# Performance work log

Measured on AMD Instinct MI355X. Metric: run time of the kernel, lower is better.

## Reference

```python
import jax, jax.numpy as jnp
import numpy as np

D_MODEL = 256
SEQ_L = 4096
BATCH = 8
H = 3 * D_MODEL   # inner width after 3-branch concat
N_STATE = 32      # complex conjugate pairs -> d_state=64 real
KSIZES = (3, 7, 15)
DILATIONS = (1, 2, 4)


def setup_inputs() -> dict:
    k = jax.random.split(jax.random.key(0), 16)
    d = D_MODEL
    def w(ki, shape, scale):
        return jax.random.normal(ki, shape, jnp.float32) * scale
    inp = {"x": jax.random.normal(k[0], (BATCH, SEQ_L, d), jnp.float32)}
    for i, ksz in enumerate(KSIZES):
        inp[f"conv_w{i}"] = w(k[1 + i], (d, d, ksz), (d * ksz) ** -0.5)
        inp[f"conv_b{i}"] = jnp.zeros((d,), jnp.float32)
    inp["gate_w"] = w(k[4], (H, d), d ** -0.5)
    inp["gate_b"] = jnp.zeros((H,), jnp.float32)
    inp["res_w"] = w(k[5], (H, d), d ** -0.5)
    inp["res_b"] = jnp.zeros((H,), jnp.float32)
    # S4D (diagonal SSM) parameters, d_state=64 -> 32 complex pairs
    inp["log_dt"] = jax.random.uniform(k[6], (H,), jnp.float32, np.log(0.001), np.log(0.1))
    inp["A_re"] = -0.5 * jnp.ones((H, N_STATE), jnp.float32)
    inp["A_im"] = jnp.broadcast_to(np.pi * jnp.arange(N_STATE, dtype=jnp.float32), (H, N_STATE)).copy()
    inp["C_re"] = w(k[7], (H, N_STATE), 0.2)
    inp["C_im"] = w(k[8], (H, N_STATE), 0.2)
    inp["Dskip"] = jax.random.normal(k[9], (H,), jnp.float32)
    inp["ln_gamma"] = jnp.ones((H,), jnp.float32)
    inp["ln_beta"] = jnp.zeros((H,), jnp.float32)
    return inp


def _dil_conv(u, w, b, dil):
    # u: [B, C, L], w: [O, I, K], torch 'same' padding (odd kernels)
    y = jax.lax.conv_general_dilated(
        u, w, window_strides=(1,), padding="SAME", rhs_dilation=(dil,),
        dimension_numbers=("NCH", "OIH", "NCH"))
    return y + b[None, :, None]


def _s4d_apply(u, log_dt, A_re, A_im, C_re, C_im, Dskip):
    # u: [B, H, L]; diagonal SSM long convolution via FFT (ZOH discretization)
    L = u.shape[-1]
    dt = jnp.exp(log_dt)                          # [H]
    A = A_re + 1j * A_im                          # [H, N]
    C = C_re + 1j * C_im                          # [H, N]
    dtA = dt[:, None] * A                         # [H, N]
    C_disc = C * (jnp.exp(dtA) - 1.0) / A         # ZOH input matrix folded into C
    t = jnp.arange(L, dtype=jnp.float32)
    vand = jnp.exp(dtA[:, :, None] * t)           # [H, N, L] Vandermonde
    kern = 2.0 * jnp.real(jnp.einsum("hn,hnl->hl", C_disc, vand))  # [H, L]
    n_fft = 2 * L
    kf = jnp.fft.rfft(kern, n_fft)                # [H, n_fft/2+1]
    uf = jnp.fft.rfft(u, n_fft)                   # [B, H, n_fft/2+1]
    y = jnp.fft.irfft(uf * kf[None], n_fft)[..., :L]
    return y + Dskip[None, :, None] * u


def reference(x, conv_w0, conv_b0, conv_w1, conv_b1, conv_w2, conv_b2,
              gate_w, gate_b, res_w, res_b,
              log_dt, A_re, A_im, C_re, C_im, Dskip, ln_gamma, ln_beta):
    u = jnp.transpose(x, (0, 2, 1))               # [B, d, L]
    convs = [
        _dil_conv(u, conv_w0, conv_b0, DILATIONS[0]),
        _dil_conv(u, conv_w1, conv_b1, DILATIONS[1]),
        _dil_conv(u, conv_w2, conv_b2, DILATIONS[2]),
    ]
    combined = jnp.concatenate(convs, axis=1)     # [B, 3d, L]
    gate = jax.nn.sigmoid(jnp.einsum("bdl,od->bol", u, gate_w) + gate_b[None, :, None])
    gated = combined * gate
    s4_out = _s4d_apply(gated, log_dt, A_re, A_im, C_re, C_im, Dskip)
    resid = jnp.einsum("bdl,od->bol", u, res_w) + res_b[None, :, None]
    out = jnp.transpose(s4_out + resid, (0, 2, 1))  # [B, L, 3d]
    mu = jnp.mean(out, axis=-1, keepdims=True)
    var = jnp.mean((out - mu) ** 2, axis=-1, keepdims=True)
    return (out - mu) * jax.lax.rsqrt(var + 1e-5) * ln_gamma + ln_beta
```

## Files before the change

kernel.cpp:

```cpp
#include <hip/hip_runtime.h>
#include <cstdint>
#include <cstddef>


#define B_ 8
#define L_ 4096
#define D_ 256
#define H_ 768
#define NST 32
#define LC 128
#define NC 32

typedef _Float16 f16;
typedef _Float16 f16x8 __attribute__((ext_vector_type(8)));
typedef _Float16 f16x4 __attribute__((ext_vector_type(4)));
typedef float f32x4 __attribute__((ext_vector_type(4)));

__device__ __forceinline__ f32x4 mfma16(f16x8 a, f16x8 b, f32x4 c) {
  return __builtin_amdgcn_mfma_f32_16x16x32_f16(a, b, c, 0, 0, 0);
}

#define GLDS16(g, l)                                                              \
  __builtin_amdgcn_global_load_lds((const __attribute__((address_space(1))) void*)(g), \
                                   (__attribute__((address_space(3))) void*)(l), 16, 0, 0)


__global__ __launch_bounds__(256) void cast4(const float* __restrict__ s, f16* __restrict__ d) {
  int i = (blockIdx.x * 256 + threadIdx.x) * 4;
  float4 x = *(const float4*)(s + i);
  d[i + 0] = (f16)x.x; d[i + 1] = (f16)x.y; d[i + 2] = (f16)x.z; d[i + 3] = (f16)x.w;
}

__global__ __launch_bounds__(256) void zfill(float* __restrict__ z) {
  z[threadIdx.x] = 0.f;
}

__global__ __launch_bounds__(256) void prep_convA(const float* __restrict__ w0,
                                                  const float* __restrict__ w1,
                                                  const float* __restrict__ w2,
                                                  f16* __restrict__ A) {
  int idx = blockIdx.x * 256 + threadIdx.x;
  const int n0 = 256 * 256 * 3, n1 = 256 * 256 * 7;
  const float* w; int K, base;
  if (idx < n0) { w = w0; K = 3; base = 0; }
  else if (idx < n0 + n1) { idx -= n0; w = w1; K = 7; base = 256 * 768; }
  else { idx -= n0 + n1; w = w2; K = 15; base = 256 * 768 + 256 * 1792; }
  int o = idx / (256 * K); int r = idx - o * (256 * K); int j = r / K; int t = r - j * K;
  A[base + o * (256 * K) + t * 256 + j] = (f16)w[idx];
}

__global__ __launch_bounds__(256) void s4_params(const float* __restrict__ log_dt,
                                                 const float* __restrict__ A_re,
                                                 const float* __restrict__ A_im,
                                                 const float* __restrict__ C_re,
                                                 const float* __restrict__ C_im,
                                                 f16* __restrict__ A1, f16* __restrict__ A2,
                                                 float* __restrict__ WLc) {
  int idx = blockIdx.x * 256 + threadIdx.x;
  int h = idx >> 5, n = idx & 31;
  float dt = expf(log_dt[h]);
  float Ar = A_re[idx], Ai = A_im[idx];
  float ar = dt * Ar, ai = dt * Ai;
  float e = expf(ar), sn, cs; sincosf(ai, &sn, &cs);
  float wr = e * cs, wi = e * sn;
  float den = Ar * Ar + Ai * Ai;
  float Er = wr - 1.f, Ei = wi;
  float Cr = C_re[idx], Ci = C_im[idx];
  float nr = Cr * Er - Ci * Ei, ni = Cr * Ei + Ci * Er;
  float Cdr = (nr * Ar + ni * Ai) / den;
  float Cdi = (ni * Ar - nr * Ai) / den;
  f16* A1r = A1 + ((size_t)h * 64 + 2 * n) * LC;
  f16* A1i = A1 + ((size_t)h * 64 + 2 * n + 1) * LC;
  float pr = 1.f, pi = 0.f;
  for (int j = 0; j < LC; ++j) {
    A1r[LC - 1 - j] = (f16)pr; A1i[LC - 1 - j] = (f16)pi;
    float t0 = pr * wr - pi * wi; pi = pr * wi + pi * wr; pr = t0;
  }
  WLc[idx * 2] = pr; WLc[idx * 2 + 1] = pi;
  float qr = wr, qi = wi;
  for (int t = 0; t < LC; ++t) {
    A2[((size_t)h * LC + t) * 64 + 2 * n]     = (f16)(2.f * (Cdr * qr - Cdi * qi));
    A2[((size_t)h * LC + t) * 64 + 2 * n + 1] = (f16)(-2.f * (Cdr * qi + Cdi * qr));
    float t0 = qr * wr - qi * wi; qi = qr * wi + qi * wr; qr = t0;
  }
}

__global__ __launch_bounds__(256) void s4_kernelvec(const float* __restrict__ log_dt,
                                                    const float* __restrict__ A_re,
                                                    const float* __restrict__ A_im,
                                                    const float* __restrict__ C_re,
                                                    const float* __restrict__ C_im,
                                                    float* __restrict__ kT) {
  int idx = blockIdx.x * 256 + threadIdx.x;
  int h = idx >> 7, j = idx & 127;
  float dt = expf(log_dt[h]);
  float acc = 0.f;
  for (int n = 0; n < NST; ++n) {
    float Ar = A_re[h * 32 + n], Ai = A_im[h * 32 + n];
    float ar = dt * Ar, ai = dt * Ai;
    float e1 = expf(ar), s1, c1; sincosf(ai, &s1, &c1);
    float wr = e1 * c1, wi = e1 * s1;
    float den = Ar * Ar + Ai * Ai;
    float Er = wr - 1.f, Ei = wi;
    float Cr = C_re[h * 32 + n], Ci = C_im[h * 32 + n];
    float nr = Cr * Er - Ci * Ei, ni = Cr * Ei + Ci * Er;
    float Cdr = (nr * Ar + ni * Ai) / den, Cdi = (ni * Ar - nr * Ai) / den;
    float ej = expf(ar * (float)j), sj, cj; sincosf(ai * (float)j, &sj, &cj);
    acc += 2.f * (Cdr * (ej * cj) - Cdi * (ej * sj));
  }
  kT[idx] = acc;
}

__global__ __launch_bounds__(256) void gemm_gr(
    const f16* __restrict__ xh, const f16* __restrict__ Agr,
    const float* __restrict__ gate_b, const float* __restrict__ res_b,
    f16* __restrict__ gts, f16* __restrict__ res) {
  __shared__ f16 As[128 * 64];
  __shared__ f16 Bs[128 * 64];
  const int mt = blockIdx.y, nt = blockIdx.x;
  const int b = nt >> 5, l0 = (nt & 31) * 128;
  const bool isg = mt < 6;
  const int hbase = (isg ? mt : mt - 6) * 128;
  const f16* Abase = Agr + (size_t)((isg ? 0 : 768) + hbase) * 256;
  const int tid = threadIdx.x;
  const int wid = tid >> 6, lane = tid & 63, l15 = lane & 15, quad = lane >> 4;
  const int wm = (wid & 1) * 64, wn = (wid >> 1) * 64;
  const int srow = (wid << 5) + (lane >> 3);
  const int sperm = ((lane & 7) ^ (lane >> 3)) << 3;
  char* AsL = (char*)As + (wid << 12);
  char* BsL = (char*)Bs + (wid << 12);
  const f16* xrow = xh + (((size_t)b * L_) << 8);

  f32x4 acc[4][4];
#pragma unroll
  for (int i = 0; i < 4; ++i)
#pragma unroll
    for (int j = 0; j < 4; ++j) acc[i][j] = (f32x4){0.f, 0.f, 0.f, 0.f};

  for (int kc = 0; kc < 4; ++kc) {
#pragma unroll
    for (int j = 0; j < 4; ++j) {
      int row = srow + j * 8;
      GLDS16(Abase + (size_t)row * 256 + kc * 64 + sperm, AsL + (j << 10));
      GLDS16(xrow + ((size_t)(l0 + row) << 8) + kc * 64 + sperm, BsL + (j << 10));
    }
    __syncthreads();
#pragma unroll
    for (int k2 = 0; k2 < 2; ++k2) {
      f16x8 af[4], bf[4];
#pragma unroll
      for (int mi = 0; mi < 4; ++mi) {
        int r = wm + mi * 16 + l15;
        af[mi] = *(const f16x8*)(&As[r * 64 + (((k2 * 4 + quad) ^ (r & 7)) << 3)]);
      }
#pragma unroll
      for (int ni = 0; ni < 4; ++ni) {
        int r = wn + ni * 16 + l15;
        bf[ni] = *(const f16x8*)(&Bs[r * 64 + (((k2 * 4 + quad) ^ (r & 7)) << 3)]);
      }
#pragma unroll
      for (int mi = 0; mi < 4; ++mi)
#pragma unroll
        for (int ni = 0; ni < 4; ++ni) acc[mi][ni] = mfma16(af[mi], bf[ni], acc[mi][ni]);
    }
    __syncthreads();
  }

  if (isg) {
#pragma unroll
    for (int mi = 0; mi < 4; ++mi)
#pragma unroll
      for (int ni = 0; ni < 4; ++ni) {
        int hg = hbase + wm + mi * 16 + quad * 4;
        int lg = l0 + wn + ni * 16 + l15;
#pragma unroll
        for (int r = 0; r < 4; ++r) {
          float val = acc[mi][ni][r] + gate_b[hg + r];
          gts[((size_t)(b * H_ + hg + r)) * L_ + lg] = (f16)(1.f / (1.f + expf(-val)));
        }
      }
  } else {
#pragma unroll
    for (int mi = 0; mi < 4; ++mi)
#pragma unroll
      for (int ni = 0; ni < 4; ++ni) {
        int hg = hbase + wm + mi * 16 + quad * 4;
        int lg = l0 + wn + ni * 16 + l15;
#pragma unroll
        for (int r = 0; r < 4; ++r)
          res[((size_t)(b * H_ + hg + r)) * L_ + lg] = (f16)(acc[mi][ni][r] + res_b[hg + r]);
      }
  }
}

__global__ __launch_bounds__(256) void gemm_conv(
    const f16* __restrict__ xh, const f16* __restrict__ Aconv,
    const float* __restrict__ cb0, const float* __restrict__ cb1, const float* __restrict__ cb2,
    const f16* __restrict__ gts, const f16* __restrict__ zbuf,
    f16* __restrict__ v) {
  __shared__ f16 As[128 * 64];
  __shared__ f16 Bs[128 * 64];
  const int mt = blockIdx.y, nt = blockIdx.x;
  const int b = nt >> 5, l0 = (nt & 31) * 128;
  const int ci = 2 - (mt >> 1);
  const int m0 = (mt & 1) * 128;
  const int tid = threadIdx.x;
  const int wid = tid >> 6, lane = tid & 63, l15 = lane & 15, quad = lane >> 4;
  const int wm = (wid & 1) * 64, wn = (wid >> 1) * 64;
  const int srow = (wid << 5) + (lane >> 3);
  const int sperm = ((lane & 7) ^ (lane >> 3)) << 3;
  char* AsL = (char*)As + (wid << 12);
  char* BsL = (char*)Bs + (wid << 12);
  const f16* xrow = xh + (((size_t)b * L_) << 8);

  const f16* Acb; int Krow, taps, dil;
  if (ci == 0)      { Acb = Aconv;                          Krow = 768;  taps = 3;  dil = 1; }
  else if (ci == 1) { Acb = Aconv + 256 * 768;              Krow = 1792; taps = 7;  dil = 2; }
  else              { Acb = Aconv + 256 * 768 + 256 * 1792; Krow = 3840; taps = 15; dil = 4; }

  f32x4 acc[4][4];
#pragma unroll
  for (int i = 0; i < 4; ++i)
#pragma unroll
    for (int j = 0; j < 4; ++j) acc[i][j] = (f32x4){0.f, 0.f, 0.f, 0.f};

  for (int t = 0; t < taps; ++t) {
    const f16* Arows = Acb + (size_t)m0 * Krow + t * 256;
    int boff = (t - (taps - 1) / 2) * dil;
    for (int kc = 0; kc < 4; ++kc) {
#pragma unroll
      for (int j = 0; j < 4; ++j) {
        int row = srow + j * 8;
        GLDS16(Arows + (size_t)row * Krow + kc * 64 + sperm, AsL + (j << 10));
        int gl = l0 + row + boff;
        const f16* gb = xrow + ((size_t)gl << 8) + kc * 64 + sperm;
        if (gl < 0 || gl >= L_) gb = zbuf;
        GLDS16(gb, BsL + (j << 10));
      }
      __syncthreads();
#pragma unroll
      for (int k2 = 0; k2 < 2; ++k2) {
        f16x8 af[4], bf[4];
#pragma unroll
        for (int mi = 0; mi < 4; ++mi) {
          int r = wm + mi * 16 + l15;
          af[mi] = *(const f16x8*)(&As[r * 64 + (((k2 * 4 + quad) ^ (r & 7)) << 3)]);
        }
#pragma unroll
        for (int ni = 0; ni < 4; ++ni) {
          int r = wn + ni * 16 + l15;
          bf[ni] = *(const f16x8*)(&Bs[r * 64 + (((k2 * 4 + quad) ^ (r & 7)) << 3)]);
        }
#pragma unroll
        for (int mi = 0; mi < 4; ++mi)
#pragma unroll
          for (int ni = 0; ni < 4; ++ni) acc[mi][ni] = mfma16(af[mi], bf[ni], acc[mi][ni]);
      }
      __syncthreads();
    }
  }

  const float* cbias = (ci == 0) ? cb0 : (ci == 1 ? cb1 : cb2);
#pragma unroll
  for (int mi = 0; mi < 4; ++mi)
#pragma unroll
    for (int ni = 0; ni < 4; ++ni) {
      int mg = m0 + wm + mi * 16 + quad * 4;
      int lg = l0 + wn + ni * 16 + l15;
#pragma unroll
      for (int r = 0; r < 4; ++r) {
        size_t a = ((size_t)(b * H_ + ci * 256 + mg + r)) * L_ + lg;
        float val = (acc[mi][ni][r] + cbias[mg + r]) * (float)gts[a];
        v[a] = (f16)val;
      }
    }
}

__global__ __launch_bounds__(256) void s1_states(const f16* __restrict__ v,
                                                 const f16* __restrict__ A1,
                                                 float* __restrict__ Xend) {
  __shared__ f16 A1s[64 * 136];
  __shared__ f16 Vs[128 * 136];
  const int h = blockIdx.y, cb = blockIdx.x;
  const int tid = threadIdx.x;
  {
    int row = tid >> 2, q = tid & 3;
    const f16x8* src = (const f16x8*)(A1 + ((size_t)h * 64 + row) * 128 + q * 32);
    f16x8* dst = (f16x8*)(&A1s[row * 136 + q * 32]);
    dst[0] = src[0]; dst[1] = src[1]; dst[2] = src[2]; dst[3] = src[3];
  }
  {
    int col = tid >> 1, half = tid & 1;
    int cg = cb * 128 + col, b = cg >> 5, c = cg & 31;
    const f16x8* src = (const f16x8*)(v + ((size_t)(b * H_ + h)) * L_ + c * 128 + half * 64);
    f16x8* dst = (f16x8*)(&Vs[col * 136 + half * 64]);
    dst[0] = src[0]; dst[1] = src[1]; dst[2] = src[2]; dst[3] = src[3];
    dst[4] = src[4]; dst[5] = src[5]; dst[6] = src[6]; dst[7] = src[7];
  }
  __syncthreads();
  const int wid = tid >> 6, lane = tid & 63, l15 = lane & 15, quad = lane >> 4;
  const int n0 = wid * 32;
  f32x4 acc[4][2];
#pragma unroll
  for (int i = 0; i < 4; ++i) { acc[i][0] = (f32x4){0,0,0,0}; acc[i][1] = (f32x4){0,0,0,0}; }
#pragma unroll
  for (int bk = 0; bk < 4; ++bk) {
    f16x8 af[4], bf[2];
#pragma unroll
    for (int mi = 0; mi < 4; ++mi)
      af[mi] = *(const f16x8*)(&A1s[(mi * 16 + l15) * 136 + bk * 32 + quad * 8]);
#pragma unroll
    for (int ni = 0; ni < 2; ++ni)
      bf[ni] = *(const f16x8*)(&Vs[(n0 + ni * 16 + l15) * 136 + bk * 32 + quad * 8]);
#pragma unroll
    for (int mi = 0; mi < 4; ++mi)
#pragma unroll
      for (int ni = 0; ni < 2; ++ni) acc[mi][ni] = mfma16(af[mi], bf[ni], acc[mi][ni]);
  }
#pragma unroll
  for (int mi = 0; mi < 4; ++mi)
#pragma unroll
    for (int ni = 0; ni < 2; ++ni) {
      int cg = cb * 128 + n0 + ni * 16 + l15, b = cg >> 5, c = cg & 31;
      float* dst = Xend + (((size_t)(b * H_ + h)) * NC + c) * 64 + mi * 16 + quad * 4;
      *(f32x4*)dst = acc[mi][ni];
    }
}

__global__ __launch_bounds__(256) void s2_scan(float* __restrict__ X, const float* __restrict__ WLc) {
  int idx = blockIdx.x * 256 + threadIdx.x;
  int n = idx & 31, bh = idx >> 5, h = bh % H_;
  float Wr = WLc[(h * NST + n) * 2], Wi = WLc[(h * NST + n) * 2 + 1];
  float xr = 0.f, xi = 0.f;
  float* base = X + (size_t)bh * NC * 64 + 2 * n;
  for (int c = 0; c < NC; ++c) {
    float er = base[c * 64], ei = base[c * 64 + 1];
    base[c * 64] = xr; base[c * 64 + 1] = xi;
    float t = Wr * xr - Wi * xi + er;
    xi = Wr * xi + Wi * xr + ei; xr = t;
  }
}

__global__ __launch_bounds__(256) void s3_output(const f16* __restrict__ v,
                                                 const f16* __restrict__ A2g,
                                                 const f16* __restrict__ res,
                                                 const float* __restrict__ kT,
                                                 const float* __restrict__ Xin,
                                                 const float* __restrict__ Dskip,
                                                 f16* __restrict__ y4) {
  __shared__ f16 Ts[128 * 136];
  __shared__ f16 Vs[64 * 136];
  __shared__ float kTs[128];
  f16* A2s = Ts;
  f16* Xs = Ts + 128 * 72;
  const int h = blockIdx.y, cb = blockIdx.x;
  const int tid = threadIdx.x;
  if (tid < 128) kTs[tid] = kT[h * 128 + tid];
  {
    int col = tid >> 2, q = tid & 3;
    int cg = cb * 64 + col, b = cg >> 5, c = cg & 31;
    const f16x8* src = (const f16x8*)(v + ((size_t)(b * H_ + h)) * L_ + c * 128 + q * 32);
    f16x8* dst = (f16x8*)(&Vs[col * 136 + q * 32]);
    dst[0] = src[0]; dst[1] = src[1]; dst[2] = src[2]; dst[3] = src[3];
  }
  __syncthreads();
  {
    int tau = tid >> 1, h64 = (tid & 1) * 64;
#pragma unroll
    for (int jv = 0; jv < 8; ++jv) {
      int s0 = h64 + jv * 8;
      f16x8 w;
#pragma unroll
      for (int e = 0; e < 8; ++e) {
        int s = s0 + e;
        w[e] = (f16)((s <= tau) ? kTs[tau - s] : 0.f);
      }
      *(f16x8*)(&Ts[tau * 136 + s0]) = w;
    }
  }
  __syncthreads();
  const int wid = tid >> 6, lane = tid & 63, l15 = lane & 15, quad = lane >> 4;
  const int wm = (wid & 1) * 64, wn = (wid >> 1) * 32;
  f32x4 acc[4][2];
#pragma unroll
  for (int i = 0; i < 4; ++i) { acc[i][0] = (f32x4){0,0,0,0}; acc[i][1] = (f32x4){0,0,0,0}; }
#pragma unroll
  for (int bk = 0; bk < 4; ++bk) {
    f16x8 af[4], bf[2];
#pragma unroll
    for (int mi = 0; mi < 4; ++mi)
      af[mi] = *(const f16x8*)(&Ts[(wm + mi * 16 + l15) * 136 + bk * 32 + quad * 8]);
#pragma unroll
    for (int ni = 0; ni < 2; ++ni)
      bf[ni] = *(const f16x8*)(&Vs[(wn + ni * 16 + l15) * 136 + bk * 32 + quad * 8]);
#pragma unroll
    for (int mi = 0; mi < 4; ++mi)
#pragma unroll
      for (int ni = 0; ni < 2; ++ni) acc[mi][ni] = mfma16(af[mi], bf[ni], acc[mi][ni]);
  }
  __syncthreads();
  {
    int row = tid >> 1, half = tid & 1;
    const f16x8* src = (const f16x8*)(A2g + ((size_t)h * 128 + row) * 64 + half * 32);
    f16x8* dst = (f16x8*)(&A2s[row * 72 + half * 32]);
    dst[0] = src[0]; dst[1] = src[1]; dst[2] = src[2]; dst[3] = src[3];
  }
  {
    int col = tid >> 2, part = tid & 3;
    int cg = cb * 64 + col, b = cg >> 5, c = cg & 31;
    const f32x4* src = (const f32x4*)(Xin + (((size_t)(b * H_ + h)) * NC + c) * 64 + part * 16);
    f16* dst = Xs + col * 72 + part * 16;
#pragma unroll
    for (int j = 0; j < 4; ++j) {
      f32x4 x = src[j];
      dst[j * 4 + 0] = (f16)x[0]; dst[j * 4 + 1] = (f16)x[1];
      dst[j * 4 + 2] = (f16)x[2]; dst[j * 4 + 3] = (f16)x[3];
    }
  }
  __syncthreads();
#pragma unroll
  for (int bk = 0; bk < 2; ++bk) {
    f16x8 af[4], bf[2];
#pragma unroll
    for (int mi = 0; mi < 4; ++mi)
      af[mi] = *(const f16x8*)(&A2s[(wm + mi * 16 + l15) * 72 + bk * 32 + quad * 8]);
#pragma unroll
    for (int ni = 0; ni < 2; ++ni)
      bf[ni] = *(const f16x8*)(&Xs[(wn + ni * 16 + l15) * 72 + bk * 32 + quad * 8]);
#pragma unroll
    for (int mi = 0; mi < 4; ++mi)
#pragma unroll
      for (int ni = 0; ni < 2; ++ni) acc[mi][ni] = mfma16(af[mi], bf[ni], acc[mi][ni]);
  }
  float Dh = Dskip[h];
#pragma unroll
  for (int mi = 0; mi < 4; ++mi)
#pragma unroll
    for (int ni = 0; ni < 2; ++ni) {
      int col = wn + ni * 16 + l15;
      int cg = cb * 64 + col, b = cg >> 5, c = cg & 31;
      int tau0 = wm + mi * 16 + quad * 4;
      size_t lbase = ((size_t)(b * H_ + h)) * L_ + c * 128 + tau0;
      const f16* rp = res + lbase;
      f16x4 o;
#pragma unroll
      for (int r = 0; r < 4; ++r)
        o[r] = (f16)(acc[mi][ni][r] + Dh * (float)Vs[col * 136 + tau0 + r] + (float)rp[r]);
      *(f16x4*)(y4 + lbase) = o;
    }
}

__global__ __launch_bounds__(256) void layernorm_t(const f16* __restrict__ y4,
                                                   const float* __restrict__ gamma,
                                                   const float* __restrict__ beta,
                                                   float* __restrict__ out) {
  __shared__ f16 Ys[768 * 72];
  __shared__ float psum[256], psq[256], mu[64], rs[64];
  const int b = blockIdx.y, l0 = blockIdx.x * 64;
  const int tid = threadIdx.x;
  {
    int r8 = tid >> 3, c = tid & 7;
    for (int it = 0; it < 24; ++it) {
      int hh = it * 32 + r8;
      f16x8 x = *(const f16x8*)(y4 + ((size_t)(b * H_ + hh)) * L_ + l0 + c * 8);
      *(f16x8*)(&Ys[hh * 72 + c * 8]) = x;
    }
  }
  __syncthreads();
  {
    int l = tid & 63, hg = tid >> 6;
    float s = 0.f, s2 = 0.f;
    for (int k = 0; k < 192; ++k) {
      float val = (float)Ys[(hg * 192 + k) * 72 + l];
      s += val; s2 += val * val;
    }
    psum[hg * 64 + l] = s; psq[hg * 64 + l] = s2;
  }
  __syncthreads();
  if (tid < 64) {
    float S = 0.f, S2 = 0.f;
    for (int g = 0; g < 4; ++g) { S += psum[g * 64 + tid]; S2 += psq[g * 64 + tid]; }
    float m = S / 768.f;
    float var = S2 / 768.f - m * m;
    mu[tid] = m; rs[tid] = rsqrtf(var + 1e-5f);
  }
  __syncthreads();
  float g0 = gamma[tid], g1 = gamma[256 + tid], g2 = gamma[512 + tid];
  float be0 = beta[tid], be1 = beta[256 + tid], be2 = beta[512 + tid];
  for (int lv = 0; lv < 8; ++lv) {
    f16x8 y0 = *(const f16x8*)(&Ys[(size_t)tid * 72 + lv * 8]);
    f16x8 y1 = *(const f16x8*)(&Ys[(size_t)(256 + tid) * 72 + lv * 8]);
    f16x8 y2 = *(const f16x8*)(&Ys[(size_t)(512 + tid) * 72 + lv * 8]);
#pragma unroll
    for (int e = 0; e < 8; ++e) {
      int ll = lv * 8 + e;
      float m = mu[ll], r = rs[ll];
      size_t ob = ((size_t)b * L_ + l0 + ll) * H_;
      out[ob + tid]       = ((float)y0[e] - m) * r * g0 + be0;
      out[ob + 256 + tid] = ((float)y1[e] - m) * r * g1 + be1;
      out[ob + 512 + tid] = ((float)y2[e] - m) * r * g2 + be2;
    }
  }
}

extern "C" void kernel_launch(void* const* d_in, const int* in_sizes, int n_in,
                              void* d_out, int out_size, void* d_ws, size_t ws_size,
                              hipStream_t stream) {
  const float* x      = (const float*)d_in[0];
  const float* cw0    = (const float*)d_in[1];
  const float* cb0    = (const float*)d_in[2];
  const float* cw1    = (const float*)d_in[3];
  const float* cb1    = (const float*)d_in[4];
  const float* cw2    = (const float*)d_in[5];
  const float* cb2    = (const float*)d_in[6];
  const float* gate_w = (const float*)d_in[7];
  const float* gate_b = (const float*)d_in[8];
  const float* res_w  = (const float*)d_in[9];
  const float* res_b  = (const float*)d_in[10];
  const float* log_dt = (const float*)d_in[11];
  const float* A_re   = (const float*)d_in[12];
  const float* A_im   = (const float*)d_in[13];
  const float* C_re   = (const float*)d_in[14];
  const float* C_im   = (const float*)d_in[15];
  const float* Dskip  = (const float*)d_in[16];
  const float* ln_g   = (const float*)d_in[17];
  const float* ln_b   = (const float*)d_in[18];
  float* out = (float*)d_out;

  char* ws = (char*)d_ws;
  f16*   xh   = (f16*)(ws + 0);
  f16*   Ac   = (f16*)(ws + 16777216);
  f16*   Ag   = (f16*)(ws + 20054016);
  f16*   zbuf = (f16*)(ws + 20840448);
  f16*   vb   = (f16*)(ws + 20841472);
  f16*   resb = (f16*)(ws + 71173120);
  f16*   gts  = (f16*)(ws + 121504768);
  f16*   A1   = (f16*)(ws + 171836416);
  f16*   A2   = (f16*)(ws + 184419328);
  float* kT   = (float*)(ws + 197002240);
  float* WLc  = (float*)(ws + 197395456);
  float* Xe   = (float*)(ws + 197592064);
  f16*   y4   = (f16*)(ws + 247923712);

  cast4<<<8192, 256, 0, stream>>>(x, xh);
  cast4<<<192, 256, 0, stream>>>(gate_w, Ag);
  cast4<<<192, 256, 0, stream>>>(res_w, Ag + 768 * 256);
  zfill<<<1, 256, 0, stream>>>((float*)zbuf);
  prep_convA<<<6400, 256, 0, stream>>>(cw0, cw1, cw2, Ac);
  s4_params<<<96, 256, 0, stream>>>(log_dt, A_re, A_im, C_re, C_im, A1, A2, WLc);
  s4_kernelvec<<<384, 256, 0, stream>>>(log_dt, A_re, A_im, C_re, C_im, kT);

  gemm_gr<<<dim3(256, 12), 256, 0, stream>>>(xh, Ag, gate_b, res_b, gts, resb);
  gemm_conv<<<dim3(256, 6), 256, 0, stream>>>(xh, Ac, cb0, cb1, cb2, gts, zbuf, vb);

  s1_states<<<dim3(2, 768), 256, 0, stream>>>(vb, A1, Xe);
  s2_scan<<<768, 256, 0, stream>>>(Xe, WLc);
  s3_output<<<dim3(4, 768), 256, 0, stream>>>(vb, A2, resb, kT, Xe, Dskip, y4);

  layernorm_t<<<dim3(64, 8), 256, 0, stream>>>(y4, ln_g, ln_b, out);
}
```

Measured before the change: 502.6 us.

## Fuse prep and S4 param kernels, fold chunk scan into s1 with fp16 states

Merges the cast, zero-fill and conv-weight reorder kernels into one launch, and the two S4 parameter kernels into another, cutting launch count. The separate s2_scan pass is removed: s1_states stages its chunk-end states in LDS and runs the inter-chunk complex recurrence locally, writing prefix states directly as fp16. This drops a full fp32 read-modify-write of the state buffer and lets s3 load fp16 states without conversion. It costs some precision on the stored states and leaves only 128 threads active during the serial scan.

```diff
diff --git a/kernel.cpp b/kernel.cpp
--- a/kernel.cpp
+++ b/kernel.cpp
@@ -14,6 +14,7 @@
 typedef _Float16 f16;
 typedef _Float16 f16x8 __attribute__((ext_vector_type(8)));
 typedef _Float16 f16x4 __attribute__((ext_vector_type(4)));
+typedef _Float16 f16x2 __attribute__((ext_vector_type(2)));
 typedef float f32x4 __attribute__((ext_vector_type(4)));
 
 __device__ __forceinline__ f32x4 mfma16(f16x8 a, f16x8 b, f32x4 c) {
@@ -24,91 +25,97 @@
   __builtin_amdgcn_global_load_lds((const __attribute__((address_space(1))) void*)(g), \
                                    (__attribute__((address_space(3))) void*)(l), 16, 0, 0)
 
-
-__global__ __launch_bounds__(256) void cast4(const float* __restrict__ s, f16* __restrict__ d) {
-  int i = (blockIdx.x * 256 + threadIdx.x) * 4;
-  float4 x = *(const float4*)(s + i);
-  d[i + 0] = (f16)x.x; d[i + 1] = (f16)x.y; d[i + 2] = (f16)x.z; d[i + 3] = (f16)x.w;
-}
-
-__global__ __launch_bounds__(256) void zfill(float* __restrict__ z) {
-  z[threadIdx.x] = 0.f;
-}
-
-__global__ __launch_bounds__(256) void prep_convA(const float* __restrict__ w0,
-                                                  const float* __restrict__ w1,
-                                                  const float* __restrict__ w2,
-                                                  f16* __restrict__ A) {
-  int idx = blockIdx.x * 256 + threadIdx.x;
-  const int n0 = 256 * 256 * 3, n1 = 256 * 256 * 7;
-  const float* w; int K, base;
-  if (idx < n0) { w = w0; K = 3; base = 0; }
-  else if (idx < n0 + n1) { idx -= n0; w = w1; K = 7; base = 256 * 768; }
-  else { idx -= n0 + n1; w = w2; K = 15; base = 256 * 768 + 256 * 1792; }
-  int o = idx / (256 * K); int r = idx - o * (256 * K); int j = r / K; int t = r - j * K;
-  A[base + o * (256 * K) + t * 256 + j] = (f16)w[idx];
-}
-
-__global__ __launch_bounds__(256) void s4_params(const float* __restrict__ log_dt,
-                                                 const float* __restrict__ A_re,
-                                                 const float* __restrict__ A_im,
-                                                 const float* __restrict__ C_re,
-                                                 const float* __restrict__ C_im,
-                                                 f16* __restrict__ A1, f16* __restrict__ A2,
-                                                 float* __restrict__ WLc) {
-  int idx = blockIdx.x * 256 + threadIdx.x;
-  int h = idx >> 5, n = idx & 31;
-  float dt = expf(log_dt[h]);
-  float Ar = A_re[idx], Ai = A_im[idx];
-  float ar = dt * Ar, ai = dt * Ai;
-  float e = expf(ar), sn, cs; sincosf(ai, &sn, &cs);
-  float wr = e * cs, wi = e * sn;
-  float den = Ar * Ar + Ai * Ai;
-  float Er = wr - 1.f, Ei = wi;
-  float Cr = C_re[idx], Ci = C_im[idx];
-  float nr = Cr * Er - Ci * Ei, ni = Cr * Ei + Ci * Er;
-  float Cdr = (nr * Ar + ni * Ai) / den;
-  float Cdi = (ni * Ar - nr * Ai) / den;
-  f16* A1r = A1 + ((size_t)h * 64 + 2 * n) * LC;
-  f16* A1i = A1 + ((size_t)h * 64 + 2 * n + 1) * LC;
-  float pr = 1.f, pi = 0.f;
-  for (int j = 0; j < LC; ++j) {
-    A1r[LC - 1 - j] = (f16)pr; A1i[LC - 1 - j] = (f16)pi;
-    float t0 = pr * wr - pi * wi; pi = pr * wi + pi * wr; pr = t0;
-  }
-  WLc[idx * 2] = pr; WLc[idx * 2 + 1] = pi;
-  float qr = wr, qi = wi;
-  for (int t = 0; t < LC; ++t) {
-    A2[((size_t)h * LC + t) * 64 + 2 * n]     = (f16)(2.f * (Cdr * qr - Cdi * qi));
-    A2[((size_t)h * LC + t) * 64 + 2 * n + 1] = (f16)(-2.f * (Cdr * qi + Cdi * qr));
-    float t0 = qr * wr - qi * wi; qi = qr * wi + qi * wr; qr = t0;
-  }
-}
-
-__global__ __launch_bounds__(256) void s4_kernelvec(const float* __restrict__ log_dt,
-                                                    const float* __restrict__ A_re,
-                                                    const float* __restrict__ A_im,
-                                                    const float* __restrict__ C_re,
-                                                    const float* __restrict__ C_im,
-                                                    float* __restrict__ kT) {
-  int idx = blockIdx.x * 256 + threadIdx.x;
-  int h = idx >> 7, j = idx & 127;
-  float dt = expf(log_dt[h]);
-  float acc = 0.f;
-  for (int n = 0; n < NST; ++n) {
-    float Ar = A_re[h * 32 + n], Ai = A_im[h * 32 + n];
+__global__ __launch_bounds__(256) void prep_all(
+    const float* __restrict__ x, const float* __restrict__ gate_w,
+    const float* __restrict__ res_w,
+    const float* __restrict__ w0, const float* __restrict__ w1, const float* __restrict__ w2,
+    f16* __restrict__ xh, f16* __restrict__ Ag, float* __restrict__ zbuf,
+    f16* __restrict__ A) {
+  int bid = blockIdx.x, tid = threadIdx.x;
+  if (bid < 8192) {
+    int i = (bid * 256 + tid) * 4;
+    float4 v = *(const float4*)(x + i);
+    xh[i+0]=(f16)v.x; xh[i+1]=(f16)v.y; xh[i+2]=(f16)v.z; xh[i+3]=(f16)v.w;
+  } else if (bid < 8384) {
+    int i = ((bid - 8192) * 256 + tid) * 4;
+    float4 v = *(const float4*)(gate_w + i);
+    Ag[i+0]=(f16)v.x; Ag[i+1]=(f16)v.y; Ag[i+2]=(f16)v.z; Ag[i+3]=(f16)v.w;
+  } else if (bid < 8576) {
+    int i = ((bid - 8384) * 256 + tid) * 4;
+    float4 v = *(const float4*)(res_w + i);
+    f16* d = Ag + 768 * 256;
+    d[i+0]=(f16)v.x; d[i+1]=(f16)v.y; d[i+2]=(f16)v.z; d[i+3]=(f16)v.w;
+  } else if (bid == 8576) {
+    zbuf[tid] = 0.f;
+  } else {
+    int idx = (bid - 8577) * 256 + tid;
+    const int n0 = 256 * 256 * 3, n1 = 256 * 256 * 7;
+    const float* w; int K, base;
+    if (idx < n0) { w = w0; K = 3; base = 0; }
+    else if (idx < n0 + n1) { idx -= n0; w = w1; K = 7; base = 256 * 768; }
+    else { idx -= n0 + n1; w = w2; K = 15; base = 256 * 768 + 256 * 1792; }
+    int o = idx / (256 * K); int r = idx - o * (256 * K); int j = r / K; int t = r - j * K;
+    A[base + o * (256 * K) + t * 256 + j] = (f16)w[idx];
+  }
+}
+
+__global__ __launch_bounds__(256) void s4_all(const float* __restrict__ log_dt,
+                                              const float* __restrict__ A_re,
+                                              const float* __restrict__ A_im,
+                                              const float* __restrict__ C_re,
+                                              const float* __restrict__ C_im,
+                                              f16* __restrict__ A1, f16* __restrict__ A2,
+                                              float* __restrict__ WLc,
+                                              float* __restrict__ kT) {
+  int bid = blockIdx.x, tid = threadIdx.x;
+  if (bid < 96) {
+    int idx = bid * 256 + tid;
+    int h = idx >> 5, n = idx & 31;
+    float dt = expf(log_dt[h]);
+    float Ar = A_re[idx], Ai = A_im[idx];
     float ar = dt * Ar, ai = dt * Ai;
-    float e1 = expf(ar), s1, c1; sincosf(ai, &s1, &c1);
-    float wr = e1 * c1, wi = e1 * s1;
+    float e = expf(ar), sn, cs; sincosf(ai, &sn, &cs);
+    float wr = e * cs, wi = e * sn;
     float den = Ar * Ar + Ai * Ai;
     float Er = wr - 1.f, Ei = wi;
-    float Cr = C_re[h * 32 + n], Ci = C_im[h * 32 + n];
+    float Cr = C_re[idx], Ci = C_im[idx];
     float nr = Cr * Er - Ci * Ei, ni = Cr * Ei + Ci * Er;
-    float Cdr = (nr * Ar + ni * Ai) / den, Cdi = (ni * Ar - nr * Ai) / den;
-    float ej = expf(ar * (float)j), sj, cj; sincosf(ai * (float)j, &sj, &cj);
-    acc += 2.f * (Cdr * (ej * cj) - Cdi * (ej * sj));
-  }
-  kT[idx] = acc;
+    float Cdr = (nr * Ar + ni * Ai) / den;
+    float Cdi = (ni * Ar - nr * Ai) / den;
+    f16* A1r = A1 + ((size_t)h * 64 + 2 * n) * LC;
+    f16* A1i = A1 + ((size_t)h * 64 + 2 * n + 1) * LC;
+    float pr = 1.f, pi = 0.f;
+    for (int j = 0; j < LC; ++j) {
+      A1r[LC - 1 - j] = (f16)pr; A1i[LC - 1 - j] = (f16)pi;
+      float t0 = pr * wr - pi * wi; pi = pr * wi + pi * wr; pr = t0;
+    }
+    WLc[idx * 2] = pr; WLc[idx * 2 + 1] = pi;
+    float qr = wr, qi = wi;
+    for (int t = 0; t < LC; ++t) {
+      A2[((size_t)h * LC + t) * 64 + 2 * n]     = (f16)(2.f * (Cdr * qr - Cdi * qi));
+      A2[((size_t)h * LC + t) * 64 + 2 * n + 1] = (f16)(-2.f * (Cdr * qi + Cdi * qr));
+      float t0 = qr * wr - qi * wi; qi = qr * wi + qi * wr; qr = t0;
+    }
+  } else {
+    int idx = (bid - 96) * 256 + tid;
+    int h = idx >> 7, j = idx & 127;
+    float dt = expf(log_dt[h]);
+    float acc = 0.f;
+    for (int n = 0; n < NST; ++n) {
+      float Ar = A_re[h * 32 + n], Ai = A_im[h * 32 + n];
+      float ar = dt * Ar, ai = dt * Ai;
+      float e1 = expf(ar), s1, c1; sincosf(ai, &s1, &c1);
+      float wr = e1 * c1, wi = e1 * s1;
+      float den = Ar * Ar + Ai * Ai;
+      float Er = wr - 1.f, Ei = wi;
+      float Cr = C_re[h * 32 + n], Ci = C_im[h * 32 + n];
+      float nr = Cr * Er - Ci * Ei, ni = Cr * Ei + Ci * Er;
+      float Cdr = (nr * Ar + ni * Ai) / den, Cdi = (ni * Ar - nr * Ai) / den;
+      float ej = expf(ar * (float)j), sj, cj; sincosf(ai * (float)j, &sj, &cj);
+      acc += 2.f * (Cdr * (ej * cj) - Cdi * (ej * sj));
+    }
+    kT[idx] = acc;
+  }
 }
 
 __global__ __launch_bounds__(256) void gemm_gr(
@@ -278,7 +285,8 @@
 
 __global__ __launch_bounds__(256) void s1_states(const f16* __restrict__ v,
                                                  const f16* __restrict__ A1,
-                                                 float* __restrict__ Xend) {
+                                                 const float* __restrict__ WLc,
+                                                 f16* __restrict__ Xin) {
   __shared__ f16 A1s[64 * 136];
   __shared__ f16 Vs[128 * 136];
   const int h = blockIdx.y, cb = blockIdx.x;
@@ -317,27 +325,30 @@
 #pragma unroll
       for (int ni = 0; ni < 2; ++ni) acc[mi][ni] = mfma16(af[mi], bf[ni], acc[mi][ni]);
   }
+  __syncthreads();
+  float* Xls = (float*)Vs;
 #pragma unroll
   for (int mi = 0; mi < 4; ++mi)
 #pragma unroll
     for (int ni = 0; ni < 2; ++ni) {
-      int cg = cb * 128 + n0 + ni * 16 + l15, b = cg >> 5, c = cg & 31;
-      float* dst = Xend + (((size_t)(b * H_ + h)) * NC + c) * 64 + mi * 16 + quad * 4;
-      *(f32x4*)dst = acc[mi][ni];
-    }
-}
-
-__global__ __launch_bounds__(256) void s2_scan(float* __restrict__ X, const float* __restrict__ WLc) {
-  int idx = blockIdx.x * 256 + threadIdx.x;
-  int n = idx & 31, bh = idx >> 5, h = bh % H_;
-  float Wr = WLc[(h * NST + n) * 2], Wi = WLc[(h * NST + n) * 2 + 1];
-  float xr = 0.f, xi = 0.f;
-  float* base = X + (size_t)bh * NC * 64 + 2 * n;
-  for (int c = 0; c < NC; ++c) {
-    float er = base[c * 64], ei = base[c * 64 + 1];
-    base[c * 64] = xr; base[c * 64 + 1] = xi;
-    float t = Wr * xr - Wi * xi + er;
-    xi = Wr * xi + Wi * xr + ei; xr = t;
+      int col = n0 + ni * 16 + l15;
+      *(f32x4*)(&Xls[col * 68 + mi * 16 + quad * 4]) = acc[mi][ni];
+    }
+  __syncthreads();
+  if (tid < 128) {
+    int b4 = tid >> 5, n = tid & 31;
+    int b = cb * 4 + b4;
+    float Wr = WLc[(h * NST + n) * 2], Wi = WLc[(h * NST + n) * 2 + 1];
+    float xr = 0.f, xi = 0.f;
+    f16* xout = Xin + (((size_t)(b * H_ + h)) * NC) * 64 + 2 * n;
+    for (int c = 0; c < NC; ++c) {
+      float er = Xls[(b4 * 32 + c) * 68 + 2 * n];
+      float ei = Xls[(b4 * 32 + c) * 68 + 2 * n + 1];
+      f16x2 o; o[0] = (f16)xr; o[1] = (f16)xi;
+      *(f16x2*)(xout + (size_t)c * 64) = o;
+      float t = Wr * xr - Wi * xi + er;
+      xi = Wr * xi + Wi * xr + ei; xr = t;
+    }
   }
 }
 
@@ -345,7 +356,7 @@
                                                  const f16* __restrict__ A2g,
                                                  const f16* __restrict__ res,
                                                  const float* __restrict__ kT,
-                                                 const float* __restrict__ Xin,
+                                                 const f16* __restrict__ Xin,
                                                  const float* __restrict__ Dskip,
                                                  f16* __restrict__ y4) {
   __shared__ f16 Ts[128 * 136];
@@ -408,14 +419,9 @@
   {
     int col = tid >> 2, part = tid & 3;
     int cg = cb * 64 + col, b = cg >> 5, c = cg & 31;
-    const f32x4* src = (const f32x4*)(Xin + (((size_t)(b * H_ + h)) * NC + c) * 64 + part * 16);
-    f16* dst = Xs + col * 72 + part * 16;
-#pragma unroll
-    for (int j = 0; j < 4; ++j) {
-      f32x4 x = src[j];
-      dst[j * 4 + 0] = (f16)x[0]; dst[j * 4 + 1] = (f16)x[1];
-      dst[j * 4 + 2] = (f16)x[2]; dst[j * 4 + 3] = (f16)x[3];
-    }
+    const f16x8* src = (const f16x8*)(Xin + (((size_t)(b * H_ + h)) * NC + c) * 64 + part * 16);
+    f16x8* dst = (f16x8*)(&Xs[col * 72 + part * 16]);
+    dst[0] = src[0]; dst[1] = src[1];
   }
   __syncthreads();
 #pragma unroll
@@ -539,23 +545,18 @@
   f16*   A2   = (f16*)(ws + 184419328);
   float* kT   = (float*)(ws + 197002240);
   float* WLc  = (float*)(ws + 197395456);
-  float* Xe   = (float*)(ws + 197592064);
-  f16*   y4   = (f16*)(ws + 247923712);
-
-  cast4<<<8192, 256, 0, stream>>>(x, xh);
-  cast4<<<192, 256, 0, stream>>>(gate_w, Ag);
-  cast4<<<192, 256, 0, stream>>>(res_w, Ag + 768 * 256);
-  zfill<<<1, 256, 0, stream>>>((float*)zbuf);
-  prep_convA<<<6400, 256, 0, stream>>>(cw0, cw1, cw2, Ac);
-  s4_params<<<96, 256, 0, stream>>>(log_dt, A_re, A_im, C_re, C_im, A1, A2, WLc);
-  s4_kernelvec<<<384, 256, 0, stream>>>(log_dt, A_re, A_im, C_re, C_im, kT);
+  f16*   Xin  = (f16*)(ws + 197592064);
+  f16*   y4   = (f16*)(ws + 222757888);
+
+  prep_all<<<14977, 256, 0, stream>>>(x, gate_w, res_w, cw0, cw1, cw2,
+                                      xh, Ag, (float*)zbuf, Ac);
+  s4_all<<<480, 256, 0, stream>>>(log_dt, A_re, A_im, C_re, C_im, A1, A2, WLc, kT);
 
   gemm_gr<<<dim3(256, 12), 256, 0, stream>>>(xh, Ag, gate_b, res_b, gts, resb);
   gemm_conv<<<dim3(256, 6), 256, 0, stream>>>(xh, Ac, cb0, cb1, cb2, gts, zbuf, vb);
 
-  s1_states<<<dim3(2, 768), 256, 0, stream>>>(vb, A1, Xe);
-  s2_scan<<<768, 256, 0, stream>>>(Xe, WLc);
-  s3_output<<<dim3(4, 768), 256, 0, stream>>>(vb, A2, resb, kT, Xe, Dskip, y4);
+  s1_states<<<dim3(2, 768), 256, 0, stream>>>(vb, A1, WLc, Xin);
+  s3_output<<<dim3(4, 768), 256, 0, stream>>>(vb, A2, resb, kT, Xin, Dskip, y4);
 
   layernorm_t<<<dim3(64, 8), 256, 0, stream>>>(y4, ln_g, ln_b, out);
 }
```

After: 459.2 us. 1.09x faster.
